# Optimization experiments

Hardware: AMD Instinct MI355X
Metric: run time of the kernel (lower is better)

## Reference

```python
import math
import jax, jax.numpy as jnp
import numpy as np

D_MODEL = 1024
D_STATE = 16
D_CONV = 4
EXPAND = 2
N_MOD = 2
D_INNER = EXPAND * D_MODEL
DT_RANK = math.ceil(D_MODEL / 16)
B_SZ = 2
SEQLEN = 2048


def setup_inputs() -> dict:
    key = jax.random.key(0)
    ks = jax.random.split(key, 10)
    hidden_states = jax.random.normal(ks[0], (B_SZ, SEQLEN, D_MODEL), jnp.float32)
    modality_ids = jax.random.randint(ks[1], (B_SZ, SEQLEN), 0, N_MOD).astype(jnp.int32)
    W_in = jax.random.normal(ks[2], (N_MOD, 2 * D_INNER, D_MODEL), jnp.float32) * (D_MODEL ** -0.5)
    conv_w = jax.random.normal(ks[3], (D_INNER, D_CONV), jnp.float32) * (D_CONV ** -0.5)
    conv_b = jnp.zeros((D_INNER,), jnp.float32)
    W_x = jax.random.normal(ks[4], (N_MOD, DT_RANK + 2 * D_STATE, D_INNER), jnp.float32) * (D_INNER ** -0.5)
    dt_init_std = DT_RANK ** -0.5
    W_dt = jax.random.uniform(ks[5], (N_MOD, D_INNER, DT_RANK), jnp.float32, -dt_init_std, dt_init_std)
    # dt bias init: inverse-softplus of dt ~ LogUniform(dt_min, dt_max), per Mamba
    dt = jnp.exp(jax.random.uniform(ks[6], (N_MOD, D_INNER), jnp.float32)
                 * (math.log(0.1) - math.log(0.001)) + math.log(0.001))
    dt = jnp.maximum(dt, 1e-4)
    b_dt = dt + jnp.log(-jnp.expm1(-dt))
    A_log = jnp.log(jnp.broadcast_to(jnp.arange(1, D_STATE + 1, dtype=jnp.float32), (D_INNER, D_STATE)))
    D = jnp.ones((D_INNER,), jnp.float32)
    W_out = jax.random.normal(ks[7], (N_MOD, D_MODEL, D_INNER), jnp.float32) * (D_INNER ** -0.5)
    return dict(hidden_states=hidden_states, modality_ids=modality_ids, W_in=W_in,
                conv_w=conv_w, conv_b=conv_b, W_x=W_x, W_dt=W_dt, b_dt=b_dt,
                A_log=A_log, D=D, W_out=W_out)


def _expert_apply(x, W, ids):
    # x: [T, d_in], W: [E, d_out, d_in], ids: [T] -> per-token expert output [T, d_out]
    all_out = jnp.einsum('td,eod->teo', x, W)
    return jnp.take_along_axis(all_out, ids[:, None, None], axis=1)[:, 0, :]


def _forward(hidden_states, modality_ids, W_in, conv_w, conv_b, W_x, W_dt, b_dt, A_log, D, W_out):
    Bsz, L, d_model = hidden_states.shape
    d_inner, d_state = A_log.shape
    dt_rank = W_dt.shape[2]
    d_conv = conv_w.shape[1]
    ids = modality_ids.reshape(-1)  # [T]

    # per-modality in_proj dispatch/combine
    xz = _expert_apply(hidden_states.reshape(-1, d_model), W_in, ids)  # [T, 2*d_inner]
    xz = xz.reshape(Bsz, L, 2 * d_inner).transpose(0, 2, 1)            # [B, 2*d_inner, L]
    x, z = jnp.split(xz, 2, axis=1)                                    # [B, d_inner, L] each

    # causal depthwise conv1d (pad left d_conv-1, truncate to L) + SiLU
    xp = jnp.pad(x, ((0, 0), (0, 0), (d_conv - 1, 0)))
    xc = conv_b[None, :, None]
    for k in range(d_conv):
        xc = xc + conv_w[None, :, k:k + 1] * xp[:, :, k:k + L]
    x = jax.nn.silu(xc)

    # per-modality x_proj -> (dt, B, C)
    xt = x.transpose(0, 2, 1).reshape(-1, d_inner)                     # [T, d_inner]
    x_dbl = _expert_apply(xt, W_x, ids)
    dt, Bm, Cm = jnp.split(x_dbl, [dt_rank, dt_rank + d_state], axis=-1)

    # per-modality dt_proj (with bias), then softplus (delta_softplus=True)
    dt = _expert_apply(dt, W_dt, ids) + b_dt[ids]                      # [T, d_inner]
    dt = jax.nn.softplus(dt)

    A = -jnp.exp(A_log)                                                # [d_inner, d_state]

    # selective scan over sequence (time-major)
    dts = dt.reshape(Bsz, L, d_inner).transpose(1, 0, 2)               # [L, B, d_inner]
    Bms = Bm.reshape(Bsz, L, d_state).transpose(1, 0, 2)               # [L, B, d_state]
    Cms = Cm.reshape(Bsz, L, d_state).transpose(1, 0, 2)               # [L, B, d_state]
    xs = x.transpose(2, 0, 1)                                          # [L, B, d_inner]

    def step(state, inp):
        x_t, dt_t, B_t, C_t = inp
        dA = jnp.exp(dt_t[..., None] * A)                              # [B, d_inner, d_state]
        state = state * dA + (dt_t * x_t)[..., None] * B_t[:, None, :]
        y_t = jnp.einsum('bdn,bn->bd', state, C_t)
        return state, y_t

    init = jnp.zeros((Bsz, d_inner, d_state), jnp.float32)
    _, ys = jax.lax.scan(step, init, (xs, dts, Bms, Cms))              # ys: [L, B, d_inner]

    y = ys.transpose(1, 0, 2)                                          # [B, L, d_inner]
    y = y + x.transpose(0, 2, 1) * D[None, None, :]                    # skip D*u
    y = y * jax.nn.silu(z.transpose(0, 2, 1))                          # z gate

    # per-modality out_proj
    out = _expert_apply(y.reshape(-1, d_inner), W_out, ids)
    return out.reshape(Bsz, L, d_model)


def reference(hidden_states, modality_ids, W_in, conv_w, conv_b, W_x, W_dt, b_dt, A_log, D, W_out):
    return _forward(hidden_states, modality_ids, W_in, conv_w, conv_b, W_x, W_dt, b_dt, A_log, D, W_out)
```

## Files before the change

### kernel.cpp

```cpp
#include <hip/hip_runtime.h>
#include <hip/hip_bf16.h>
#include <math.h>

#define B_SZ 2
#define SEQLEN 2048
#define D_MODEL 1024
#define D_INNER 2048
#define D_STATE 16
#define D_CONV 4
#define DT_RANK 64
#define NTOK (B_SZ * SEQLEN)
#define XDBL 96
#define NC 32
#define LC 64
#define PADTOT (33 * 128)

typedef float f32x4 __attribute__((ext_vector_type(4)));
typedef unsigned int u32x4 __attribute__((ext_vector_type(4)));
typedef __hip_bfloat16 bf16;

__device__ __forceinline__ float siluf(float v) { return v / (1.f + __expf(-v)); }
__device__ __forceinline__ float softplusf(float v) { return (v > 20.f) ? v : log1pf(__expf(v)); }

__device__ __forceinline__ void mfma_bf16(f32x4& acc, u32x4 a, u32x4 b) {
  asm("v_mfma_f32_16x16x32_bf16 %0, %1, %2, %0" : "+v"(acc) : "v"(a), "v"(b));
}

__device__ __forceinline__ void gload16(const bf16* g, bf16* l) {
  __builtin_amdgcn_global_load_lds(
      (const __attribute__((address_space(1))) unsigned int*)g,
      (__attribute__((address_space(3))) unsigned int*)l, 16, 0, 0);
}

__global__ __launch_bounds__(1024) void k_perm(const int* __restrict__ ids, int* __restrict__ perm) {
  __shared__ int sc[1024];
  const int tid = threadIdx.x;
  int loc[4];
  int cnt = 0;
#pragma unroll
  for (int q = 0; q < 4; q++) {
    loc[q] = ids[tid * 4 + q];
    cnt += (loc[q] == 0);
  }
  sc[tid] = cnt;
  __syncthreads();
  for (int off = 1; off < 1024; off <<= 1) {
    int v = sc[tid];
    int u = (tid >= off) ? sc[tid - off] : 0;
    __syncthreads();
    sc[tid] = v + u;
    __syncthreads();
  }
  const int N0 = sc[1023];
  const int m0 = (N0 + 127) & ~127;
  const int N1 = NTOK - N0;
  for (int idx = tid; idx < PADTOT; idx += 1024)
    if ((idx >= N0 && idx < m0) || idx >= m0 + N1) perm[idx] = -1;
  int zb = sc[tid] - cnt;
#pragma unroll
  for (int q = 0; q < 4; q++) {
    int t = tid * 4 + q;
    if (loc[q] == 0) { perm[zb] = t; zb++; }
    else             { perm[m0 + (t - zb)] = t; }
  }
}

#define CVT_H   (NTOK * D_MODEL)
#define CVT_WIN (2 * 2 * D_INNER * D_MODEL)
#define CVT_WX  (2 * XDBL * D_INNER)
#define CVT_WDT (2 * D_INNER * DT_RANK)
#define CVT_WO  (2 * D_MODEL * D_INNER)
#define CVT_TOT (CVT_H + CVT_WIN + CVT_WX + CVT_WDT + CVT_WO)
__global__ __launch_bounds__(256) void k_cvtall(const float* __restrict__ h,
                                                const float* __restrict__ Win,
                                                const float* __restrict__ Wx,
                                                const float* __restrict__ Wdt,
                                                const float* __restrict__ Wout,
                                                bf16* __restrict__ hB, bf16* __restrict__ WinB,
                                                bf16* __restrict__ WxB, bf16* __restrict__ WdtB,
                                                bf16* __restrict__ WoB) {
  size_t i = ((size_t)blockIdx.x * 256 + threadIdx.x) * 8;
  const float* src; bf16* dst; size_t off;
  if (i < CVT_H)                          { src = h;    dst = hB;   off = i; }
  else if (i < CVT_H + CVT_WIN)           { src = Win;  dst = WinB; off = i - CVT_H; }
  else if (i < CVT_H + CVT_WIN + CVT_WX)  { src = Wx;   dst = WxB;  off = i - CVT_H - CVT_WIN; }
  else if (i < CVT_TOT - CVT_WO)          { src = Wdt;  dst = WdtB; off = i - CVT_H - CVT_WIN - CVT_WX; }
  else                                    { src = Wout; dst = WoB;  off = i - (CVT_TOT - CVT_WO); }
  float4 f0 = *(const float4*)&src[off];
  float4 f1 = *(const float4*)&src[off + 4];
  __align__(16) bf16 tmp[8];
  tmp[0] = __float2bfloat16(f0.x); tmp[1] = __float2bfloat16(f0.y);
  tmp[2] = __float2bfloat16(f0.z); tmp[3] = __float2bfloat16(f0.w);
  tmp[4] = __float2bfloat16(f1.x); tmp[5] = __float2bfloat16(f1.y);
  tmp[6] = __float2bfloat16(f1.z); tmp[7] = __float2bfloat16(f1.w);
  *(u32x4*)&dst[off] = *(const u32x4*)tmp;
}

template <int KDIM, int NW, int LDO, int EPI>
__global__ __launch_bounds__(256) void k_gemmG(const bf16* __restrict__ actB,
                                               const int* __restrict__ perm,
                                               const int* __restrict__ ids,
                                               const bf16* __restrict__ WB,
                                               const float* __restrict__ bias,
                                               float* __restrict__ out0,
                                               float* __restrict__ out1,
                                               bf16* __restrict__ outb) {
  __shared__ bf16 As[128 * 64];
  __shared__ bf16 Ws[128 * 64];
  __shared__ int permL[128];
  const int tid = threadIdx.x;
  const int ot = blockIdx.x * 128;
  const int tt = blockIdx.y * 128;
  if (tid < 128) permL[tid] = perm[tt + tid];

  const int lane = tid & 63, w = tid >> 6;
  const int wr = w >> 1, wc = w & 1;
  const int lr = lane & 15, lg = lane >> 4;

  const int t00 = perm[tt];
  const int eu = (t00 >= 0) ? ids[t00] : 0;
  const size_t wexp = (size_t)eu * NW * KDIM;

  const int srow = w * 32 + (lane >> 3);
  const int scol = (lane & 7) * 8;
  size_t abase[4], bbase[4];
  int ldsoff[4];
#pragma unroll
  for (int v = 0; v < 4; v++) {
    const int row = srow + v * 8;
    int ta = perm[tt + row];
    if (ta < 0) ta = 0;
    abase[v] = (size_t)ta * KDIM + scol;
    int orow = ot + row;
    if (NW % 128 != 0) orow = (orow < NW) ? orow : (NW - 1);
    bbase[v] = wexp + (size_t)orow * KDIM + scol;
    ldsoff[v] = (w * 32 + v * 8) * 64;
  }

  f32x4 acc[4][4];
#pragma unroll
  for (int i = 0; i < 4; i++)
#pragma unroll
    for (int j = 0; j < 4; j++) acc[i][j] = (f32x4){0.f, 0.f, 0.f, 0.f};

  for (int k0 = 0; k0 < KDIM; k0 += 64) {
#pragma unroll
    for (int v = 0; v < 4; v++) {
      gload16(&actB[abase[v] + k0], &As[ldsoff[v]]);
      gload16(&WB[bbase[v] + k0], &Ws[ldsoff[v]]);
    }
    __syncthreads();
#pragma unroll
    for (int ks = 0; ks < 64; ks += 32) {
      u32x4 a[4], b[4];
#pragma unroll
      for (int f = 0; f < 4; f++)
        a[f] = *(const u32x4*)&As[(wr * 64 + f * 16 + lr) * 64 + ks + lg * 8];
#pragma unroll
      for (int f = 0; f < 4; f++)
        b[f] = *(const u32x4*)&Ws[(wc * 64 + f * 16 + lr) * 64 + ks + lg * 8];
#pragma unroll
      for (int i = 0; i < 4; i++)
#pragma unroll
        for (int j = 0; j < 4; j++) mfma_bf16(acc[i][j], a[i], b[j]);
    }
    __syncthreads();
  }

#pragma unroll
  for (int i = 0; i < 4; i++) {
#pragma unroll
    for (int r = 0; r < 4; r++) {
      const int m = wr * 64 + i * 16 + lg * 4 + r;
      const int t = permL[m];
      if (t < 0) continue;
#pragma unroll
      for (int j = 0; j < 4; j++) {
        const int col = ot + wc * 64 + j * 16 + lr;
        float v = acc[i][j][r];
        if (EPI == 0) {
          out0[(size_t)t * LDO + col] = v;
        } else if (EPI == 1) {
          if (col < D_INNER) out0[(size_t)t * D_INNER + col] = v;
          else out1[(size_t)t * D_INNER + (col - D_INNER)] = v;
        } else if (EPI == 2) {
          v = softplusf(v + bias[eu * NW + col]);
          out0[(size_t)t * LDO + col] = v;
        } else {
          if (col < XDBL) out0[(size_t)t * XDBL + col] = v;
          if (col < DT_RANK) outb[(size_t)t * DT_RANK + col] = __float2bfloat16(v);
        }
      }
    }
  }
}

__global__ __launch_bounds__(256) void k_conv(const float* __restrict__ x_raw,
                                              const float* __restrict__ cw,
                                              const float* __restrict__ cb,
                                              float* __restrict__ x_act,
                                              bf16* __restrict__ xB) {
  int idx = blockIdx.x * 256 + threadIdx.x;
  int c = idx & (D_INNER - 1);
  int t = idx >> 11;
  int l = t & (SEQLEN - 1);
  int b = t >> 11;
  float acc = cb[c];
#pragma unroll
  for (int k = 0; k < D_CONV; k++) {
    int ll = l + k - (D_CONV - 1);
    if (ll >= 0)
      acc = fmaf(cw[c * D_CONV + k], x_raw[((size_t)(b * SEQLEN + ll)) * D_INNER + c], acc);
  }
  float s = siluf(acc);
  x_act[(size_t)idx] = s;
  xB[(size_t)idx] = __float2bfloat16(s);
}

__global__ __launch_bounds__(256) void k_scan_part(const float* __restrict__ x_act,
                                                   const float* __restrict__ dtb,
                                                   const float* __restrict__ xdbl,
                                                   const float* __restrict__ A_log,
                                                   float* __restrict__ F,
                                                   float* __restrict__ Sdt) {
  __shared__ float Bs[LC][D_STATE];
  const int tid = threadIdx.x;
  const int j = blockIdx.y;
  const int ch = blockIdx.x * 256 + tid;
  const int b = ch >> 11, c = ch & (D_INNER - 1);
  const int t0 = (b << 11) + j * LC;
  {
    int l = tid >> 2, q = (tid & 3) * 4;
    *(float4*)&Bs[l][q] = *(const float4*)&xdbl[(size_t)(t0 + l) * XDBL + DT_RANK + q];
  }
  float Ar[D_STATE];
#pragma unroll
  for (int n4 = 0; n4 < 4; n4++) {
    float4 a = *(const float4*)&A_log[(size_t)c * D_STATE + n4 * 4];
    Ar[n4 * 4 + 0] = -__expf(a.x); Ar[n4 * 4 + 1] = -__expf(a.y);
    Ar[n4 * 4 + 2] = -__expf(a.z); Ar[n4 * 4 + 3] = -__expf(a.w);
  }
  __syncthreads();
  float st[D_STATE];
#pragma unroll
  for (int n = 0; n < D_STATE; n++) st[n] = 0.f;
  float sdt = 0.f;
  float dtc = dtb[(size_t)t0 * D_INNER + c];
  float xc = x_act[(size_t)t0 * D_INNER + c];
  for (int l = 0; l < LC; l++) {
    float dtn = 0.f, xn = 0.f;
    if (l < LC - 1) {
      dtn = dtb[(size_t)(t0 + l + 1) * D_INNER + c];
      xn = x_act[(size_t)(t0 + l + 1) * D_INNER + c];
    }
    const float dtx = dtc * xc;
    sdt += dtc;
#pragma unroll
    for (int n = 0; n < D_STATE; n++) {
      float dA = __expf(dtc * Ar[n]);
      st[n] = fmaf(st[n], dA, dtx * Bs[l][n]);
    }
    dtc = dtn; xc = xn;
  }
  const size_t fb = ((size_t)j * NTOK + ch) * D_STATE;
#pragma unroll
  for (int n4 = 0; n4 < 4; n4++)
    *(float4*)&F[fb + n4 * 4] = make_float4(st[n4 * 4], st[n4 * 4 + 1], st[n4 * 4 + 2], st[n4 * 4 + 3]);
  Sdt[(size_t)j * NTOK + ch] = sdt;
}

__global__ __launch_bounds__(256) void k_combine(const float* __restrict__ F,
                                                 const float* __restrict__ Sdt,
                                                 const float* __restrict__ A_log,
                                                 float* __restrict__ s0) {
  const int gid = blockIdx.x * 256 + threadIdx.x;
  const int ch = gid >> 4, n = gid & 15, c = ch & (D_INNER - 1);
  const float Ar = -__expf(A_log[(size_t)c * D_STATE + n]);
  float s = 0.f;
  for (int j = 0; j < NC; j++) {
    s0[((size_t)j * NTOK + ch) * D_STATE + n] = s;
    s = fmaf(s, __expf(Ar * Sdt[(size_t)j * NTOK + ch]), F[((size_t)j * NTOK + ch) * D_STATE + n]);
  }
}

__global__ __launch_bounds__(256) void k_scan_fin(const float* __restrict__ x_act,
                                                  const float* __restrict__ dtb,
                                                  const float* __restrict__ xdbl,
                                                  const float* __restrict__ z_buf,
                                                  const float* __restrict__ A_log,
                                                  const float* __restrict__ Dp,
                                                  const float* __restrict__ s0,
                                                  bf16* __restrict__ ybuf) {
  __shared__ float Bs[LC][D_STATE];
  __shared__ float Cs[LC][D_STATE];
  const int tid = threadIdx.x;
  const int j = blockIdx.y;
  const int ch = blockIdx.x * 256 + tid;
  const int b = ch >> 11, c = ch & (D_INNER - 1);
  const int t0 = (b << 11) + j * LC;
  {
    int l = tid >> 2, q = (tid & 3) * 4;
    *(float4*)&Bs[l][q] = *(const float4*)&xdbl[(size_t)(t0 + l) * XDBL + DT_RANK + q];
    *(float4*)&Cs[l][q] = *(const float4*)&xdbl[(size_t)(t0 + l) * XDBL + DT_RANK + D_STATE + q];
  }
  float Ar[D_STATE];
#pragma unroll
  for (int n4 = 0; n4 < 4; n4++) {
    float4 a = *(const float4*)&A_log[(size_t)c * D_STATE + n4 * 4];
    Ar[n4 * 4 + 0] = -__expf(a.x); Ar[n4 * 4 + 1] = -__expf(a.y);
    Ar[n4 * 4 + 2] = -__expf(a.z); Ar[n4 * 4 + 3] = -__expf(a.w);
  }
  __syncthreads();
  float st[D_STATE];
  const size_t sb = ((size_t)j * NTOK + ch) * D_STATE;
#pragma unroll
  for (int n4 = 0; n4 < 4; n4++) {
    float4 s = *(const float4*)&s0[sb + n4 * 4];
    st[n4 * 4 + 0] = s.x; st[n4 * 4 + 1] = s.y; st[n4 * 4 + 2] = s.z; st[n4 * 4 + 3] = s.w;
  }
  const float Dc = Dp[c];
  float dtc = dtb[(size_t)t0 * D_INNER + c];
  float xc = x_act[(size_t)t0 * D_INNER + c];
  for (int l = 0; l < LC; l++) {
    float dtn = 0.f, xn = 0.f;
    if (l < LC - 1) {
      dtn = dtb[(size_t)(t0 + l + 1) * D_INNER + c];
      xn = x_act[(size_t)(t0 + l + 1) * D_INNER + c];
    }
    const float zv = z_buf[(size_t)(t0 + l) * D_INNER + c];
    const float dtx = dtc * xc;
    float y = 0.f;
#pragma unroll
    for (int n = 0; n < D_STATE; n++) {
      float dA = __expf(dtc * Ar[n]);
      st[n] = fmaf(st[n], dA, dtx * Bs[l][n]);
      y = fmaf(st[n], Cs[l][n], y);
    }
    float yv = fmaf(xc, Dc, y);
    ybuf[(size_t)(t0 + l) * D_INNER + c] = __float2bfloat16(yv * siluf(zv));
    dtc = dtn; xc = xn;
  }
}

extern "C" void kernel_launch(void* const* d_in, const int* in_sizes, int n_in,
                              void* d_out, int out_size, void* d_ws, size_t ws_size,
                              hipStream_t stream) {
  const float* h = (const float*)d_in[0];
  const int* ids = (const int*)d_in[1];
  const float* Win = (const float*)d_in[2];
  const float* cw = (const float*)d_in[3];
  const float* cb = (const float*)d_in[4];
  const float* Wx = (const float*)d_in[5];
  const float* Wdt = (const float*)d_in[6];
  const float* bdt = (const float*)d_in[7];
  const float* Alog = (const float*)d_in[8];
  const float* Dp = (const float*)d_in[9];
  const float* Wout = (const float*)d_in[10];
  float* out = (float*)d_out;

  const size_t NTD = (size_t)NTOK * D_INNER;
  float* ws = (float*)d_ws;
  float* x_act = ws + 0 * NTD;
  float* z_buf = ws + 1 * NTD;
  float* dtb_p = ws + 2 * NTD;
  float* xraw_p = ws + 3 * NTD;
  size_t cur = 4 * NTD;
  float* xdbl_p = ws + cur; cur += (size_t)NTOK * XDBL;
  float* sdt_p = ws + cur; cur += (size_t)NC * NTOK;
  int* perm = (int*)(ws + cur); cur += PADTOT;
  bf16* xB = (bf16*)(ws + cur); cur += NTD / 2;
  bf16* WoB = (bf16*)(ws + cur); cur += CVT_WO / 2;
  bf16* WxB = (bf16*)(ws + cur); cur += CVT_WX / 2;
  bf16* WdtB = (bf16*)(ws + cur); cur += CVT_WDT / 2;
  bf16* x64B = (bf16*)(ws + cur); cur += (size_t)NTOK * DT_RANK / 2;

  bf16* hB = (bf16*)x_act;
  bf16* WinB = (bf16*)dtb_p;
  float* F = xraw_p;
  bf16* yB = (bf16*)xraw_p;
  float* s0 = (float*)d_out;

  k_perm<<<1, 1024, 0, stream>>>(ids, perm);
  k_cvtall<<<CVT_TOT / 8 / 256, 256, 0, stream>>>(h, Win, Wx, Wdt, Wout, hB, WinB, WxB, WdtB, WoB);
  k_gemmG<D_MODEL, 2 * D_INNER, 0, 1>
      <<<dim3(32, 33), 256, 0, stream>>>(hB, perm, ids, WinB, nullptr, xraw_p, z_buf, nullptr);
  k_conv<<<NTD / 256, 256, 0, stream>>>(xraw_p, cw, cb, x_act, xB);
  k_gemmG<D_INNER, XDBL, XDBL, 3>
      <<<dim3(1, 33), 256, 0, stream>>>(xB, perm, ids, WxB, nullptr, xdbl_p, nullptr, x64B);
  k_gemmG<DT_RANK, D_INNER, D_INNER, 2>
      <<<dim3(16, 33), 256, 0, stream>>>(x64B, perm, ids, WdtB, bdt, dtb_p, nullptr, nullptr);
  k_scan_part<<<dim3(16, NC), 256, 0, stream>>>(x_act, dtb_p, xdbl_p, Alog, F, sdt_p);
  k_combine<<<256, 256, 0, stream>>>(F, sdt_p, Alog, s0);
  k_scan_fin<<<dim3(16, NC), 256, 0, stream>>>(x_act, dtb_p, xdbl_p, z_buf, Alog, Dp, s0, yB);
  k_gemmG<D_INNER, D_MODEL, D_MODEL, 0>
      <<<dim3(8, 33), 256, 0, stream>>>(yB, perm, ids, WoB, nullptr, out, nullptr, nullptr);
}
```

Measured before the change: 361.7 us.

## Split-K the x_proj GEMM, double-buffer LDS tiles, and swizzle block order

Measured after the change: 384.9 us. 6.4% more time.

```diff
diff --git a/kernel.cpp b/kernel.cpp
--- a/kernel.cpp
+++ b/kernel.cpp
@@ -96,21 +96,34 @@
   *(u32x4*)&dst[off] = *(const u32x4*)tmp;
 }
 
-template <int KDIM, int NW, int LDO, int EPI>
+template <int KDIM, int NW, int LDO, int EPI, int KSPLIT>
 __global__ __launch_bounds__(256) void k_gemmG(const bf16* __restrict__ actB,
                                                const int* __restrict__ perm,
                                                const int* __restrict__ ids,
                                                const bf16* __restrict__ WB,
                                                const float* __restrict__ bias,
                                                float* __restrict__ out0,
-                                               float* __restrict__ out1,
-                                               bf16* __restrict__ outb) {
-  __shared__ bf16 As[128 * 64];
-  __shared__ bf16 Ws[128 * 64];
+                                               float* __restrict__ out1) {
+  static_assert(KDIM % (64 * KSPLIT) == 0, "K split");
+  constexpr int KLEN = KDIM / KSPLIT;
+  constexpr int NT = KLEN / 64;
+  __shared__ bf16 As[2][128 * 64];
+  __shared__ bf16 Ws[2][128 * 64];
   __shared__ int permL[128];
   const int tid = threadIdx.x;
-  const int ot = blockIdx.x * 128;
-  const int tt = blockIdx.y * 128;
+
+  const int gx = gridDim.x;
+  const int nwg = gx * gridDim.y;
+  const int fid = blockIdx.y * gx + blockIdx.x;
+  const int q8 = nwg >> 3;
+  const int swz = (fid & 7) * q8 + (fid >> 3);
+  const int bx = swz % gx, by = swz / gx;
+
+  const int ot = (KSPLIT > 1) ? 0 : bx * 128;
+  const int kz = (KSPLIT > 1) ? bx : 0;
+  const int kbase = kz * KLEN;
+  const int tt = by * 128;
+
   if (tid < 128) permL[tid] = perm[tt + tid];
 
   const int lane = tid & 63, w = tid >> 6;
@@ -143,28 +156,37 @@
 #pragma unroll
     for (int j = 0; j < 4; j++) acc[i][j] = (f32x4){0.f, 0.f, 0.f, 0.f};
 
-  for (int k0 = 0; k0 < KDIM; k0 += 64) {
+  auto STAGE = [&](int buf, int k0) {
 #pragma unroll
     for (int v = 0; v < 4; v++) {
-      gload16(&actB[abase[v] + k0], &As[ldsoff[v]]);
-      gload16(&WB[bbase[v] + k0], &Ws[ldsoff[v]]);
-    }
-    __syncthreads();
+      gload16(&actB[abase[v] + k0], &As[buf][ldsoff[v]]);
+      gload16(&WB[bbase[v] + k0], &Ws[buf][ldsoff[v]]);
+    }
+  };
+
+  STAGE(0, kbase);
+  __syncthreads();
+  int cur = 0;
+  for (int t = 0; t < NT; t++) {
+    if (t + 1 < NT) STAGE(cur ^ 1, kbase + (t + 1) * 64);
+    const bf16* Ab = As[cur];
+    const bf16* Wb = Ws[cur];
 #pragma unroll
     for (int ks = 0; ks < 64; ks += 32) {
       u32x4 a[4], b[4];
 #pragma unroll
       for (int f = 0; f < 4; f++)
-        a[f] = *(const u32x4*)&As[(wr * 64 + f * 16 + lr) * 64 + ks + lg * 8];
+        a[f] = *(const u32x4*)&Ab[(wr * 64 + f * 16 + lr) * 64 + ks + lg * 8];
 #pragma unroll
       for (int f = 0; f < 4; f++)
-        b[f] = *(const u32x4*)&Ws[(wc * 64 + f * 16 + lr) * 64 + ks + lg * 8];
+        b[f] = *(const u32x4*)&Wb[(wc * 64 + f * 16 + lr) * 64 + ks + lg * 8];
 #pragma unroll
       for (int i = 0; i < 4; i++)
 #pragma unroll
         for (int j = 0; j < 4; j++) mfma_bf16(acc[i][j], a[i], b[j]);
     }
     __syncthreads();
+    cur ^= 1;
   }
 
 #pragma unroll
@@ -186,13 +208,24 @@
         } else if (EPI == 2) {
           v = softplusf(v + bias[eu * NW + col]);
           out0[(size_t)t * LDO + col] = v;
-        } else {
-          if (col < XDBL) out0[(size_t)t * XDBL + col] = v;
-          if (col < DT_RANK) outb[(size_t)t * DT_RANK + col] = __float2bfloat16(v);
+        } else if (EPI == 3) {
+          if (col < XDBL) out0[((size_t)kz * NTOK + t) * XDBL + col] = v;
         }
       }
     }
   }
+}
+
+__global__ __launch_bounds__(256) void k_xred(const float* __restrict__ part,
+                                              float* __restrict__ xdbl,
+                                              bf16* __restrict__ x64B) {
+  const int i = blockIdx.x * 256 + threadIdx.x;
+  float s = 0.f;
+#pragma unroll
+  for (int k = 0; k < 8; k++) s += part[(size_t)k * NTOK * XDBL + i];
+  xdbl[i] = s;
+  const int t = i / XDBL, col = i - t * XDBL;
+  if (col < DT_RANK) x64B[(size_t)t * DT_RANK + col] = __float2bfloat16(s);
 }
 
 __global__ __launch_bounds__(256) void k_conv(const float* __restrict__ x_raw,
@@ -376,22 +409,24 @@
 
   bf16* hB = (bf16*)x_act;
   bf16* WinB = (bf16*)dtb_p;
+  float* part = dtb_p;
   float* F = xraw_p;
   bf16* yB = (bf16*)xraw_p;
   float* s0 = (float*)d_out;
 
   k_perm<<<1, 1024, 0, stream>>>(ids, perm);
   k_cvtall<<<CVT_TOT / 8 / 256, 256, 0, stream>>>(h, Win, Wx, Wdt, Wout, hB, WinB, WxB, WdtB, WoB);
-  k_gemmG<D_MODEL, 2 * D_INNER, 0, 1>
-      <<<dim3(32, 33), 256, 0, stream>>>(hB, perm, ids, WinB, nullptr, xraw_p, z_buf, nullptr);
+  k_gemmG<D_MODEL, 2 * D_INNER, 0, 1, 1>
+      <<<dim3(32, 33), 256, 0, stream>>>(hB, perm, ids, WinB, nullptr, xraw_p, z_buf);
   k_conv<<<NTD / 256, 256, 0, stream>>>(xraw_p, cw, cb, x_act, xB);
-  k_gemmG<D_INNER, XDBL, XDBL, 3>
-      <<<dim3(1, 33), 256, 0, stream>>>(xB, perm, ids, WxB, nullptr, xdbl_p, nullptr, x64B);
-  k_gemmG<DT_RANK, D_INNER, D_INNER, 2>
-      <<<dim3(16, 33), 256, 0, stream>>>(x64B, perm, ids, WdtB, bdt, dtb_p, nullptr, nullptr);
+  k_gemmG<D_INNER, XDBL, XDBL, 3, 8>
+      <<<dim3(8, 33), 256, 0, stream>>>(xB, perm, ids, WxB, nullptr, part, nullptr);
+  k_xred<<<NTOK * XDBL / 256, 256, 0, stream>>>(part, xdbl_p, x64B);
+  k_gemmG<DT_RANK, D_INNER, D_INNER, 2, 1>
+      <<<dim3(16, 33), 256, 0, stream>>>(x64B, perm, ids, WdtB, bdt, dtb_p, nullptr);
   k_scan_part<<<dim3(16, NC), 256, 0, stream>>>(x_act, dtb_p, xdbl_p, Alog, F, sdt_p);
   k_combine<<<256, 256, 0, stream>>>(F, sdt_p, Alog, s0);
   k_scan_fin<<<dim3(16, NC), 256, 0, stream>>>(x_act, dtb_p, xdbl_p, z_buf, Alog, Dp, s0, yB);
-  k_gemmG<D_INNER, D_MODEL, D_MODEL, 0>
-      <<<dim3(8, 33), 256, 0, stream>>>(yB, perm, ids, WoB, nullptr, out, nullptr, nullptr);
-}
+  k_gemmG<D_INNER, D_MODEL, D_MODEL, 0, 1>
+      <<<dim3(8, 33), 256, 0, stream>>>(yB, perm, ids, WoB, nullptr, out, nullptr);
+}
```
